# Optimization experiments

Hardware: AMD Instinct MI355X
Metric: run time of the kernel (lower is better)

The kernel has to match this reference:

```python
import jax, jax.numpy as jnp
import numpy as np

N_FEATURES = 784   # binary tabular features (MNIST-like)
Z_DIM = 64         # latent dim fed to decoder net
BX = 256           # number of data points x
BZ = 4096          # number of latent samples / components z


def setup_inputs() -> dict:
    key = jax.random.key(0)
    k1, k2, k3 = jax.random.split(key, 3)
    x = jax.random.uniform(k1, (BX, N_FEATURES), dtype=jnp.float32)  # soft targets in [0,1)
    z = jax.random.normal(k2, (BZ, Z_DIM), dtype=jnp.float32)
    # net := Linear(Z_DIM -> 2*N_FEATURES)
    W = jax.random.normal(k3, (Z_DIM, 2 * N_FEATURES), dtype=jnp.float32) * 0.05
    b = jnp.zeros((2 * N_FEATURES,), dtype=jnp.float32)
    # chain-structured CLT: root = feature 0 (parent -1), feature i's parent is i-1
    tree = jnp.concatenate([jnp.array([-1], dtype=jnp.int32),
                            jnp.arange(N_FEATURES - 1, dtype=jnp.int32)])
    return {"x": x, "z": z, "W": W, "b": b, "tree": tree}


def reference(x, z, W, b, tree):
    F = tree.shape[0]
    # net(z) -> logits_p [Bz, F, 2]
    logits_p = (z @ W + b).reshape(-1, F, 2)
    # _preprocess_logits_p: at root, copy state-1 logit into state-0 slot
    root_mask = (tree == -1)  # [F]
    lp0 = jnp.where(root_mask[None, :], logits_p[:, :, 1], logits_p[:, :, 0])
    logits_p = jnp.stack([lp0, logits_p[:, :, 1]], axis=-1)  # [Bz, F, 2]
    # parent-conditioned selector x_cond [Bx, F, 2]
    xt = x[:, tree]  # gather parent values; -1 at root wraps (same as torch)
    x_cond = jnp.stack([1.0 - xt, xt], axis=-1)
    # bce (negative binary cross-entropy = Bernoulli log-likelihood):
    #   lls[b,i,j,k] = x[b,j]*log_sigmoid(lp[i,j,k]) + (1-x[b,j])*log_sigmoid(-lp[i,j,k])
    # (x_doubled duplicates x along k, so both k slots use x[b,j])
    # Then einsum('bijk,bjk->bij', lls, x_cond).sum(-1). Distribute x_cond to
    # avoid materializing the [Bx,Bz,F,2] lls tensor (same math, fused):
    ls = jax.nn.log_sigmoid(logits_p)     # [Bz, F, 2]
    lsn = jax.nn.log_sigmoid(-logits_p)   # [Bz, F, 2]
    a = x_cond * x[:, :, None]            # [Bx, F, 2]
    c = x_cond * (1.0 - x)[:, :, None]    # [Bx, F, 2]
    log_prob_bins = (jnp.einsum('bjk,ijk->bi', a, ls)
                     + jnp.einsum('bjk,ijk->bi', c, lsn))  # [Bx, Bz]
    return log_prob_bins
```

## Files before the change

kernel.cpp:

```cpp
#include <hip/hip_runtime.h>

#define NF   784
#define ZD   64
#define BXN  256
#define BZN  4096
#define KDIM 3136
#define LCOL 1568

typedef __attribute__((ext_vector_type(8))) short bf16x8;
typedef __attribute__((ext_vector_type(4))) float f32x4;
typedef __attribute__((ext_vector_type(8))) unsigned short ushort8;
typedef __attribute__((ext_vector_type(4))) unsigned short us4;

__device__ __forceinline__ unsigned short f2bf(float f) {
  unsigned u = __float_as_uint(f);
  u += 0x7fff + ((u >> 16) & 1);
  return (unsigned short)(u >> 16);
}

__device__ __forceinline__ unsigned pkbf(float a, float b) {
  unsigned r;
  asm("v_cvt_pk_bf16_f32 %0, %1, %2" : "=v"(r) : "v"(a), "v"(b));
  return r;
}

__global__ __launch_bounds__(256) void prep(const float* __restrict__ x,
                                            const float* __restrict__ W,
                                            const int* __restrict__ tree,
                                            unsigned short* __restrict__ Amat,
                                            unsigned short* __restrict__ Wt) {
  int bid = blockIdx.x, tid = threadIdx.x;
  if (bid < 1024) {
    int b = bid >> 2;
    int j = (bid & 3) * 256 + tid;
    if (j >= NF) return;
    float xb = x[b * NF + j];
    int idx = tree[j];
    int gidx = idx < 0 ? idx + NF : idx;
    float xt = x[b * NF + gidx];
    ushort4 v;
    v.x = f2bf((1.f - xt) * xb);
    v.y = f2bf(xt * xb);
    v.z = f2bf((1.f - xt) * (1.f - xb));
    v.w = f2bf(xt * (1.f - xb));
    *(ushort4*)&Amat[(size_t)b * KDIM + 4 * j] = v;
  } else {
    int t = (bid - 1024) * 256 + tid;
    int c = t >> 4, k0 = (t & 15) * 4;
    ushort4 o;
    o.x = f2bf(W[(k0 + 0) * LCOL + c]);
    o.y = f2bf(W[(k0 + 1) * LCOL + c]);
    o.z = f2bf(W[(k0 + 2) * LCOL + c]);
    o.w = f2bf(W[(k0 + 3) * LCOL + c]);
    *(ushort4*)&Wt[c * 64 + k0] = o;
  }
}

#define LP 40
__global__ __launch_bounds__(256) void gemm_fused(const unsigned short* __restrict__ Amat,
                                                  const float* __restrict__ z,
                                                  const unsigned short* __restrict__ Wt,
                                                  const float* __restrict__ bias,
                                                  const int* __restrict__ tree,
                                                  unsigned short* __restrict__ part) {
  __shared__ unsigned short As[2][256][LP];
  __shared__ unsigned short Bs[2][64][LP];
  int bid = blockIdx.x;
  int s = bid & 7, nt = bid >> 3;
  int n0 = nt * 64;
  int kt0 = s * 12 + (s < 2 ? s : 2);
  int nsteps = (s < 2) ? 13 : 12;
  int ktend = kt0 + nsteps;
  int tid = threadIdx.x;
  int w = tid >> 6, lane = tid & 63;
  int fr = lane & 15, hi = lane >> 4, kq = hi * 8;
  int srow = tid >> 2, scol = (tid & 3) * 8;
  const unsigned short* Ag = Amat + (size_t)srow * KDIM + scol;

  const float* zpf = z + (size_t)(n0 + w * 16 + fr) * 64 + kq;
  float4 zl0 = *(const float4*)(zpf);
  float4 zl1 = *(const float4*)(zpf + 4);
  float4 zl2 = *(const float4*)(zpf + 32);
  float4 zl3 = *(const float4*)(zpf + 36);
  union { unsigned u[4]; bf16x8 v; } Z0, Z1;
  Z0.u[0] = pkbf(zl0.x, zl0.y); Z0.u[1] = pkbf(zl0.z, zl0.w);
  Z0.u[2] = pkbf(zl1.x, zl1.y); Z0.u[3] = pkbf(zl1.z, zl1.w);
  Z1.u[0] = pkbf(zl2.x, zl2.y); Z1.u[1] = pkbf(zl2.z, zl2.w);
  Z1.u[2] = pkbf(zl3.x, zl3.y); Z1.u[3] = pkbf(zl3.z, zl3.w);
  bf16x8 zf0 = Z0.v, zf1 = Z1.v;

  f32x4 acc[4][4];
#pragma unroll
  for (int m = 0; m < 4; ++m)
#pragma unroll
    for (int n = 0; n < 4; ++n) acc[m][n] = (f32x4){0.f, 0.f, 0.f, 0.f};

  const unsigned short* wp = Wt + (size_t)(kt0 * 16 + fr) * 64 + kq;
  bf16x8 wf0 = *(const bf16x8*)wp;
  bf16x8 wf1 = *(const bf16x8*)(wp + 32);
  float4 b4  = *(const float4*)&bias[kt0 * 16 + 4 * hi];
  int2   tr2 = *(const int2*)&tree[kt0 * 8 + 2 * hi];
  int k0 = kt0 * 32;
  float4 ar0 = *(const float4*)(Ag + k0);
  float4 ar1 = *(const float4*)(Ag + (size_t)64 * KDIM + k0);
  float4 ar2 = *(const float4*)(Ag + (size_t)128 * KDIM + k0);
  float4 ar3 = *(const float4*)(Ag + (size_t)192 * KDIM + k0);

  int buf = 0;
  for (int i = 0; i < nsteps; ++i) {
    int kt = kt0 + i;
    f32x4 lacc = (f32x4){0.f, 0.f, 0.f, 0.f};
    lacc = __builtin_amdgcn_mfma_f32_16x16x32_bf16(wf0, zf0, lacc, 0, 0, 0);
    lacc = __builtin_amdgcn_mfma_f32_16x16x32_bf16(wf1, zf1, lacc, 0, 0, 0);
    int ktn = (kt + 1 < ktend) ? kt + 1 : kt;
    const unsigned short* wpn = Wt + (size_t)(ktn * 16 + fr) * 64 + kq;
    bf16x8 wfn0 = *(const bf16x8*)wpn;
    bf16x8 wfn1 = *(const bf16x8*)(wpn + 32);
    float4 b4n  = *(const float4*)&bias[ktn * 16 + 4 * hi];
    int2   tr2n = *(const int2*)&tree[ktn * 8 + 2 * hi];
    int k0n = ktn * 32;
    float4 arn0 = *(const float4*)(Ag + k0n);
    float4 arn1 = *(const float4*)(Ag + (size_t)64 * KDIM + k0n);
    float4 arn2 = *(const float4*)(Ag + (size_t)128 * KDIM + k0n);
    float4 arn3 = *(const float4*)(Ag + (size_t)192 * KDIM + k0n);
    float bb[4] = { b4.x, b4.y, b4.z, b4.w };
    int tt[2] = { tr2.x, tr2.y };
    union { unsigned u[4]; ushort8 v; } V;
#pragma unroll
    for (int p = 0; p < 2; ++p) {
      float l1 = lacc[2 * p + 1] + bb[2 * p + 1];
      float l0 = (tt[p] == -1) ? l1 : (lacc[2 * p] + bb[2 * p]);
      float e0 = __expf(-fabsf(l0)); float sp0 = __logf(1.f + e0);
      float ls0 = (l0 >= 0.f) ? -sp0 : l0 - sp0;
      float e1 = __expf(-fabsf(l1)); float sp1 = __logf(1.f + e1);
      float ls1 = (l1 >= 0.f) ? -sp1 : l1 - sp1;
      V.u[2 * p + 0] = pkbf(ls0, ls1);
      V.u[2 * p + 1] = pkbf(ls0 - l0, ls1 - l1);
    }
    *(float4*)&As[buf][srow      ][scol] = ar0;
    *(float4*)&As[buf][srow +  64][scol] = ar1;
    *(float4*)&As[buf][srow + 128][scol] = ar2;
    *(float4*)&As[buf][srow + 192][scol] = ar3;
    *(ushort8*)&Bs[buf][w * 16 + fr][kq] = V.v;
    __syncthreads();
    bf16x8 a[4], b[4];
#pragma unroll
    for (int m = 0; m < 4; ++m) a[m] = *(const bf16x8*)&As[buf][w * 64 + m * 16 + fr][kq];
#pragma unroll
    for (int n = 0; n < 4; ++n) b[n] = *(const bf16x8*)&Bs[buf][n * 16 + fr][kq];
#pragma unroll
    for (int m = 0; m < 4; ++m)
#pragma unroll
      for (int n = 0; n < 4; ++n)
        acc[m][n] = __builtin_amdgcn_mfma_f32_16x16x32_bf16(a[m], b[n], acc[m][n], 0, 0, 0);
    wf0 = wfn0; wf1 = wfn1; b4 = b4n; tr2 = tr2n;
    ar0 = arn0; ar1 = arn1; ar2 = arn2; ar3 = arn3;
    buf ^= 1;
  }
  int col = lane & 15, rq = hi * 4;
  unsigned short* Pp = part + (size_t)s * (256 * 4096) + (size_t)(w * 64) * 4096 + n0;
#pragma unroll
  for (int m = 0; m < 4; ++m)
#pragma unroll
    for (int n = 0; n < 4; ++n)
#pragma unroll
      for (int r = 0; r < 4; ++r)
        __builtin_nontemporal_store(f2bf(acc[m][n][r]),
                                    &Pp[(m * 16 + rq + r) * 4096 + n * 16 + col]);
}

__global__ __launch_bounds__(256) void reduce8(const unsigned short* __restrict__ part,
                                               float* __restrict__ out) {
  int t = blockIdx.x * 256 + threadIdx.x;
  f32x4 s = (f32x4){0.f, 0.f, 0.f, 0.f};
#pragma unroll
  for (int q = 0; q < 8; ++q) {
    const us4* p = (const us4*)&part[(size_t)q * (256 * 4096) + (size_t)t * 4];
    us4 v = __builtin_nontemporal_load(p);
    s[0] += __uint_as_float((unsigned)v[0] << 16);
    s[1] += __uint_as_float((unsigned)v[1] << 16);
    s[2] += __uint_as_float((unsigned)v[2] << 16);
    s[3] += __uint_as_float((unsigned)v[3] << 16);
  }
  f32x4* o = (f32x4*)&out[(size_t)t * 4];
  __builtin_nontemporal_store(s, o);
}

extern "C" void kernel_launch(void* const* d_in, const int* in_sizes, int n_in,
                              void* d_out, int out_size, void* d_ws, size_t ws_size,
                              hipStream_t stream) {
  const float* x    = (const float*)d_in[0];
  const float* z    = (const float*)d_in[1];
  const float* W    = (const float*)d_in[2];
  const float* bias = (const float*)d_in[3];
  const int*   tree = (const int*)d_in[4];
  float* out = (float*)d_out;

  unsigned short* Amat = (unsigned short*)d_ws;
  unsigned short* Wt   = (unsigned short*)((char*)d_ws + 1605632);
  unsigned short* part = (unsigned short*)((char*)d_ws + 1806336);

  prep<<<dim3(1122), 256, 0, stream>>>(x, W, tree, Amat, Wt);
  gemm_fused<<<dim3(512), 256, 0, stream>>>(Amat, z, Wt, bias, tree, part);
  reduce8<<<dim3(1024), 256, 0, stream>>>(part, out);
}
```

Measured before the change: 37.06 us.

## Double gemm block to 512 threads, halving per-wave M tile with producer waves

```diff
diff --git a/kernel.cpp b/kernel.cpp
--- a/kernel.cpp
+++ b/kernel.cpp
@@ -57,12 +57,12 @@
 }
 
 #define LP 40
-__global__ __launch_bounds__(256) void gemm_fused(const unsigned short* __restrict__ Amat,
-                                                  const float* __restrict__ z,
-                                                  const unsigned short* __restrict__ Wt,
-                                                  const float* __restrict__ bias,
-                                                  const int* __restrict__ tree,
-                                                  unsigned short* __restrict__ part) {
+__global__ __launch_bounds__(512, 4) void gemm_fused(const unsigned short* __restrict__ Amat,
+                                                     const float* __restrict__ z,
+                                                     const unsigned short* __restrict__ Wt,
+                                                     const float* __restrict__ bias,
+                                                     const int* __restrict__ tree,
+                                                     unsigned short* __restrict__ part) {
   __shared__ unsigned short As[2][256][LP];
   __shared__ unsigned short Bs[2][64][LP];
   int bid = blockIdx.x;
@@ -74,93 +74,105 @@
   int tid = threadIdx.x;
   int w = tid >> 6, lane = tid & 63;
   int fr = lane & 15, hi = lane >> 4, kq = hi * 8;
-  int srow = tid >> 2, scol = (tid & 3) * 8;
+  int srow = tid >> 1, scol = (tid & 1) * 8;
   const unsigned short* Ag = Amat + (size_t)srow * KDIM + scol;
-
-  const float* zpf = z + (size_t)(n0 + w * 16 + fr) * 64 + kq;
-  float4 zl0 = *(const float4*)(zpf);
-  float4 zl1 = *(const float4*)(zpf + 4);
-  float4 zl2 = *(const float4*)(zpf + 32);
-  float4 zl3 = *(const float4*)(zpf + 36);
-  union { unsigned u[4]; bf16x8 v; } Z0, Z1;
-  Z0.u[0] = pkbf(zl0.x, zl0.y); Z0.u[1] = pkbf(zl0.z, zl0.w);
-  Z0.u[2] = pkbf(zl1.x, zl1.y); Z0.u[3] = pkbf(zl1.z, zl1.w);
-  Z1.u[0] = pkbf(zl2.x, zl2.y); Z1.u[1] = pkbf(zl2.z, zl2.w);
-  Z1.u[2] = pkbf(zl3.x, zl3.y); Z1.u[3] = pkbf(zl3.z, zl3.w);
-  bf16x8 zf0 = Z0.v, zf1 = Z1.v;
-
-  f32x4 acc[4][4];
-#pragma unroll
-  for (int m = 0; m < 4; ++m)
+  bool prod = (w < 4);
+
+  bf16x8 zf0 = {}, zf1 = {};
+  if (prod) {
+    const float* zpf = z + (size_t)(n0 + w * 16 + fr) * 64 + kq;
+    float4 zl0 = *(const float4*)(zpf);
+    float4 zl1 = *(const float4*)(zpf + 4);
+    float4 zl2 = *(const float4*)(zpf + 32);
+    float4 zl3 = *(const float4*)(zpf + 36);
+    union { unsigned u[4]; bf16x8 v; } Z0, Z1;
+    Z0.u[0] = pkbf(zl0.x, zl0.y); Z0.u[1] = pkbf(zl0.z, zl0.w);
+    Z0.u[2] = pkbf(zl1.x, zl1.y); Z0.u[3] = pkbf(zl1.z, zl1.w);
+    Z1.u[0] = pkbf(zl2.x, zl2.y); Z1.u[1] = pkbf(zl2.z, zl2.w);
+    Z1.u[2] = pkbf(zl3.x, zl3.y); Z1.u[3] = pkbf(zl3.z, zl3.w);
+    zf0 = Z0.v; zf1 = Z1.v;
+  }
+
+  f32x4 acc[2][4];
+#pragma unroll
+  for (int m = 0; m < 2; ++m)
 #pragma unroll
     for (int n = 0; n < 4; ++n) acc[m][n] = (f32x4){0.f, 0.f, 0.f, 0.f};
 
-  const unsigned short* wp = Wt + (size_t)(kt0 * 16 + fr) * 64 + kq;
-  bf16x8 wf0 = *(const bf16x8*)wp;
-  bf16x8 wf1 = *(const bf16x8*)(wp + 32);
-  float4 b4  = *(const float4*)&bias[kt0 * 16 + 4 * hi];
-  int2   tr2 = *(const int2*)&tree[kt0 * 8 + 2 * hi];
+  bf16x8 wf0 = {}, wf1 = {};
+  float4 b4 = {};
+  int2 tr2 = {};
+  if (prod) {
+    const unsigned short* wp = Wt + (size_t)(kt0 * 16 + fr) * 64 + kq;
+    wf0 = *(const bf16x8*)wp;
+    wf1 = *(const bf16x8*)(wp + 32);
+    b4  = *(const float4*)&bias[kt0 * 16 + 4 * hi];
+    tr2 = *(const int2*)&tree[kt0 * 8 + 2 * hi];
+  }
   int k0 = kt0 * 32;
   float4 ar0 = *(const float4*)(Ag + k0);
-  float4 ar1 = *(const float4*)(Ag + (size_t)64 * KDIM + k0);
-  float4 ar2 = *(const float4*)(Ag + (size_t)128 * KDIM + k0);
-  float4 ar3 = *(const float4*)(Ag + (size_t)192 * KDIM + k0);
+  float4 ar1 = *(const float4*)(Ag + 16 + k0);
 
   int buf = 0;
   for (int i = 0; i < nsteps; ++i) {
     int kt = kt0 + i;
+    int ktn = (kt + 1 < ktend) ? kt + 1 : kt;
     f32x4 lacc = (f32x4){0.f, 0.f, 0.f, 0.f};
-    lacc = __builtin_amdgcn_mfma_f32_16x16x32_bf16(wf0, zf0, lacc, 0, 0, 0);
-    lacc = __builtin_amdgcn_mfma_f32_16x16x32_bf16(wf1, zf1, lacc, 0, 0, 0);
-    int ktn = (kt + 1 < ktend) ? kt + 1 : kt;
-    const unsigned short* wpn = Wt + (size_t)(ktn * 16 + fr) * 64 + kq;
-    bf16x8 wfn0 = *(const bf16x8*)wpn;
-    bf16x8 wfn1 = *(const bf16x8*)(wpn + 32);
-    float4 b4n  = *(const float4*)&bias[ktn * 16 + 4 * hi];
-    int2   tr2n = *(const int2*)&tree[ktn * 8 + 2 * hi];
+    if (prod) {
+      lacc = __builtin_amdgcn_mfma_f32_16x16x32_bf16(wf0, zf0, lacc, 0, 0, 0);
+      lacc = __builtin_amdgcn_mfma_f32_16x16x32_bf16(wf1, zf1, lacc, 0, 0, 0);
+    }
+    bf16x8 wfn0 = {}, wfn1 = {};
+    float4 b4n = {};
+    int2 tr2n = {};
+    if (prod) {
+      const unsigned short* wpn = Wt + (size_t)(ktn * 16 + fr) * 64 + kq;
+      wfn0 = *(const bf16x8*)wpn;
+      wfn1 = *(const bf16x8*)(wpn + 32);
+      b4n  = *(const float4*)&bias[ktn * 16 + 4 * hi];
+      tr2n = *(const int2*)&tree[ktn * 8 + 2 * hi];
+    }
     int k0n = ktn * 32;
     float4 arn0 = *(const float4*)(Ag + k0n);
-    float4 arn1 = *(const float4*)(Ag + (size_t)64 * KDIM + k0n);
-    float4 arn2 = *(const float4*)(Ag + (size_t)128 * KDIM + k0n);
-    float4 arn3 = *(const float4*)(Ag + (size_t)192 * KDIM + k0n);
-    float bb[4] = { b4.x, b4.y, b4.z, b4.w };
-    int tt[2] = { tr2.x, tr2.y };
-    union { unsigned u[4]; ushort8 v; } V;
-#pragma unroll
-    for (int p = 0; p < 2; ++p) {
-      float l1 = lacc[2 * p + 1] + bb[2 * p + 1];
-      float l0 = (tt[p] == -1) ? l1 : (lacc[2 * p] + bb[2 * p]);
-      float e0 = __expf(-fabsf(l0)); float sp0 = __logf(1.f + e0);
-      float ls0 = (l0 >= 0.f) ? -sp0 : l0 - sp0;
-      float e1 = __expf(-fabsf(l1)); float sp1 = __logf(1.f + e1);
-      float ls1 = (l1 >= 0.f) ? -sp1 : l1 - sp1;
-      V.u[2 * p + 0] = pkbf(ls0, ls1);
-      V.u[2 * p + 1] = pkbf(ls0 - l0, ls1 - l1);
-    }
-    *(float4*)&As[buf][srow      ][scol] = ar0;
-    *(float4*)&As[buf][srow +  64][scol] = ar1;
-    *(float4*)&As[buf][srow + 128][scol] = ar2;
-    *(float4*)&As[buf][srow + 192][scol] = ar3;
-    *(ushort8*)&Bs[buf][w * 16 + fr][kq] = V.v;
+    float4 arn1 = *(const float4*)(Ag + 16 + k0n);
+    if (prod) {
+      float bb[4] = { b4.x, b4.y, b4.z, b4.w };
+      int tt[2] = { tr2.x, tr2.y };
+      union { unsigned u[4]; ushort8 v; } V;
+#pragma unroll
+      for (int p = 0; p < 2; ++p) {
+        float l1 = lacc[2 * p + 1] + bb[2 * p + 1];
+        float l0 = (tt[p] == -1) ? l1 : (lacc[2 * p] + bb[2 * p]);
+        float e0 = __expf(-fabsf(l0)); float sp0 = __logf(1.f + e0);
+        float ls0 = (l0 >= 0.f) ? -sp0 : l0 - sp0;
+        float e1 = __expf(-fabsf(l1)); float sp1 = __logf(1.f + e1);
+        float ls1 = (l1 >= 0.f) ? -sp1 : l1 - sp1;
+        V.u[2 * p + 0] = pkbf(ls0, ls1);
+        V.u[2 * p + 1] = pkbf(ls0 - l0, ls1 - l1);
+      }
+      *(ushort8*)&Bs[buf][w * 16 + fr][kq] = V.v;
+    }
+    *(float4*)&As[buf][srow][scol     ] = ar0;
+    *(float4*)&As[buf][srow][scol + 16] = ar1;
     __syncthreads();
-    bf16x8 a[4], b[4];
-#pragma unroll
-    for (int m = 0; m < 4; ++m) a[m] = *(const bf16x8*)&As[buf][w * 64 + m * 16 + fr][kq];
+    bf16x8 a0 = *(const bf16x8*)&As[buf][w * 32 + fr][kq];
+    bf16x8 a1 = *(const bf16x8*)&As[buf][w * 32 + 16 + fr][kq];
+    bf16x8 b[4];
 #pragma unroll
     for (int n = 0; n < 4; ++n) b[n] = *(const bf16x8*)&Bs[buf][n * 16 + fr][kq];
 #pragma unroll
-    for (int m = 0; m < 4; ++m)
-#pragma unroll
-      for (int n = 0; n < 4; ++n)
-        acc[m][n] = __builtin_amdgcn_mfma_f32_16x16x32_bf16(a[m], b[n], acc[m][n], 0, 0, 0);
+    for (int n = 0; n < 4; ++n) {
+      acc[0][n] = __builtin_amdgcn_mfma_f32_16x16x32_bf16(a0, b[n], acc[0][n], 0, 0, 0);
+      acc[1][n] = __builtin_amdgcn_mfma_f32_16x16x32_bf16(a1, b[n], acc[1][n], 0, 0, 0);
+    }
     wf0 = wfn0; wf1 = wfn1; b4 = b4n; tr2 = tr2n;
-    ar0 = arn0; ar1 = arn1; ar2 = arn2; ar3 = arn3;
+    ar0 = arn0; ar1 = arn1;
     buf ^= 1;
   }
   int col = lane & 15, rq = hi * 4;
-  unsigned short* Pp = part + (size_t)s * (256 * 4096) + (size_t)(w * 64) * 4096 + n0;
-#pragma unroll
-  for (int m = 0; m < 4; ++m)
+  unsigned short* Pp = part + (size_t)s * (256 * 4096) + (size_t)(w * 32) * 4096 + n0;
+#pragma unroll
+  for (int m = 0; m < 2; ++m)
 #pragma unroll
     for (int n = 0; n < 4; ++n)
 #pragma unroll
@@ -201,6 +213,6 @@
   unsigned short* part = (unsigned short*)((char*)d_ws + 1806336);
 
   prep<<<dim3(1122), 256, 0, stream>>>(x, W, tree, Amat, Wt);
-  gemm_fused<<<dim3(512), 256, 0, stream>>>(Amat, z, Wt, bias, tree, part);
+  gemm_fused<<<dim3(512), 512, 0, stream>>>(Amat, z, Wt, bias, tree, part);
   reduce8<<<dim3(1024), 256, 0, stream>>>(part, out);
 }
```

Measured after the change: 41.18 us. 1.11x slower.

## Software-pipeline decoder logits and log-sigmoid one K-step ahead of main MFMA

Applied to the files above, without the earlier changes.

```diff
diff --git a/kernel.cpp b/kernel.cpp
--- a/kernel.cpp
+++ b/kernel.cpp
@@ -95,37 +95,19 @@
 #pragma unroll
     for (int n = 0; n < 4; ++n) acc[m][n] = (f32x4){0.f, 0.f, 0.f, 0.f};
 
-  const unsigned short* wp = Wt + (size_t)(kt0 * 16 + fr) * 64 + kq;
-  bf16x8 wf0 = *(const bf16x8*)wp;
-  bf16x8 wf1 = *(const bf16x8*)(wp + 32);
-  float4 b4  = *(const float4*)&bias[kt0 * 16 + 4 * hi];
-  int2   tr2 = *(const int2*)&tree[kt0 * 8 + 2 * hi];
-  int k0 = kt0 * 32;
-  float4 ar0 = *(const float4*)(Ag + k0);
-  float4 ar1 = *(const float4*)(Ag + (size_t)64 * KDIM + k0);
-  float4 ar2 = *(const float4*)(Ag + (size_t)128 * KDIM + k0);
-  float4 ar3 = *(const float4*)(Ag + (size_t)192 * KDIM + k0);
-
-  int buf = 0;
-  for (int i = 0; i < nsteps; ++i) {
-    int kt = kt0 + i;
+  ushort8 V;
+  {
+    const unsigned short* wpp = Wt + (size_t)(kt0 * 16 + fr) * 64 + kq;
+    bf16x8 pwf0 = *(const bf16x8*)wpp;
+    bf16x8 pwf1 = *(const bf16x8*)(wpp + 32);
+    float4 pb4  = *(const float4*)&bias[kt0 * 16 + 4 * hi];
+    int2   ptr2 = *(const int2*)&tree[kt0 * 8 + 2 * hi];
     f32x4 lacc = (f32x4){0.f, 0.f, 0.f, 0.f};
-    lacc = __builtin_amdgcn_mfma_f32_16x16x32_bf16(wf0, zf0, lacc, 0, 0, 0);
-    lacc = __builtin_amdgcn_mfma_f32_16x16x32_bf16(wf1, zf1, lacc, 0, 0, 0);
-    int ktn = (kt + 1 < ktend) ? kt + 1 : kt;
-    const unsigned short* wpn = Wt + (size_t)(ktn * 16 + fr) * 64 + kq;
-    bf16x8 wfn0 = *(const bf16x8*)wpn;
-    bf16x8 wfn1 = *(const bf16x8*)(wpn + 32);
-    float4 b4n  = *(const float4*)&bias[ktn * 16 + 4 * hi];
-    int2   tr2n = *(const int2*)&tree[ktn * 8 + 2 * hi];
-    int k0n = ktn * 32;
-    float4 arn0 = *(const float4*)(Ag + k0n);
-    float4 arn1 = *(const float4*)(Ag + (size_t)64 * KDIM + k0n);
-    float4 arn2 = *(const float4*)(Ag + (size_t)128 * KDIM + k0n);
-    float4 arn3 = *(const float4*)(Ag + (size_t)192 * KDIM + k0n);
-    float bb[4] = { b4.x, b4.y, b4.z, b4.w };
-    int tt[2] = { tr2.x, tr2.y };
-    union { unsigned u[4]; ushort8 v; } V;
+    lacc = __builtin_amdgcn_mfma_f32_16x16x32_bf16(pwf0, zf0, lacc, 0, 0, 0);
+    lacc = __builtin_amdgcn_mfma_f32_16x16x32_bf16(pwf1, zf1, lacc, 0, 0, 0);
+    float bb[4] = { pb4.x, pb4.y, pb4.z, pb4.w };
+    int tt[2] = { ptr2.x, ptr2.y };
+    union { unsigned u[4]; ushort8 v; } VV;
 #pragma unroll
     for (int p = 0; p < 2; ++p) {
       float l1 = lacc[2 * p + 1] + bb[2 * p + 1];
@@ -134,25 +116,72 @@
       float ls0 = (l0 >= 0.f) ? -sp0 : l0 - sp0;
       float e1 = __expf(-fabsf(l1)); float sp1 = __logf(1.f + e1);
       float ls1 = (l1 >= 0.f) ? -sp1 : l1 - sp1;
-      V.u[2 * p + 0] = pkbf(ls0, ls1);
-      V.u[2 * p + 1] = pkbf(ls0 - l0, ls1 - l1);
+      VV.u[2 * p + 0] = pkbf(ls0, ls1);
+      VV.u[2 * p + 1] = pkbf(ls0 - l0, ls1 - l1);
     }
+    V = VV.v;
+  }
+  int k0 = kt0 * 32;
+  float4 ar0 = *(const float4*)(Ag + k0);
+  float4 ar1 = *(const float4*)(Ag + (size_t)64 * KDIM + k0);
+  float4 ar2 = *(const float4*)(Ag + (size_t)128 * KDIM + k0);
+  float4 ar3 = *(const float4*)(Ag + (size_t)192 * KDIM + k0);
+  int kt1 = (kt0 + 1 < ktend) ? kt0 + 1 : ktend - 1;
+  const unsigned short* wp1 = Wt + (size_t)(kt1 * 16 + fr) * 64 + kq;
+  bf16x8 wf0 = *(const bf16x8*)wp1;
+  bf16x8 wf1 = *(const bf16x8*)(wp1 + 32);
+  float4 b4  = *(const float4*)&bias[kt1 * 16 + 4 * hi];
+  int2   tr2 = *(const int2*)&tree[kt1 * 8 + 2 * hi];
+
+  int buf = 0;
+  for (int i = 0; i < nsteps; ++i) {
+    int kt = kt0 + i;
+    int ktn  = (kt + 1 < ktend) ? kt + 1 : ktend - 1;
+    int ktnn = (kt + 2 < ktend) ? kt + 2 : ktend - 1;
     *(float4*)&As[buf][srow      ][scol] = ar0;
     *(float4*)&As[buf][srow +  64][scol] = ar1;
     *(float4*)&As[buf][srow + 128][scol] = ar2;
     *(float4*)&As[buf][srow + 192][scol] = ar3;
-    *(ushort8*)&Bs[buf][w * 16 + fr][kq] = V.v;
+    *(ushort8*)&Bs[buf][w * 16 + fr][kq] = V;
+    int k0n = ktn * 32;
+    float4 arn0 = *(const float4*)(Ag + k0n);
+    float4 arn1 = *(const float4*)(Ag + (size_t)64 * KDIM + k0n);
+    float4 arn2 = *(const float4*)(Ag + (size_t)128 * KDIM + k0n);
+    float4 arn3 = *(const float4*)(Ag + (size_t)192 * KDIM + k0n);
     __syncthreads();
     bf16x8 a[4], b[4];
 #pragma unroll
     for (int m = 0; m < 4; ++m) a[m] = *(const bf16x8*)&As[buf][w * 64 + m * 16 + fr][kq];
 #pragma unroll
     for (int n = 0; n < 4; ++n) b[n] = *(const bf16x8*)&Bs[buf][n * 16 + fr][kq];
+    f32x4 lacc = (f32x4){0.f, 0.f, 0.f, 0.f};
+    lacc = __builtin_amdgcn_mfma_f32_16x16x32_bf16(wf0, zf0, lacc, 0, 0, 0);
+    lacc = __builtin_amdgcn_mfma_f32_16x16x32_bf16(wf1, zf1, lacc, 0, 0, 0);
+    const unsigned short* wpn = Wt + (size_t)(ktnn * 16 + fr) * 64 + kq;
+    bf16x8 wfn0 = *(const bf16x8*)wpn;
+    bf16x8 wfn1 = *(const bf16x8*)(wpn + 32);
+    float4 b4n  = *(const float4*)&bias[ktnn * 16 + 4 * hi];
+    int2   tr2n = *(const int2*)&tree[ktnn * 8 + 2 * hi];
+    float bb[4] = { b4.x, b4.y, b4.z, b4.w };
+    int tt[2] = { tr2.x, tr2.y };
+    union { unsigned u[4]; ushort8 v; } VV;
+#pragma unroll
+    for (int p = 0; p < 2; ++p) {
+      float l1 = lacc[2 * p + 1] + bb[2 * p + 1];
+      float l0 = (tt[p] == -1) ? l1 : (lacc[2 * p] + bb[2 * p]);
+      float e0 = __expf(-fabsf(l0)); float sp0 = __logf(1.f + e0);
+      float ls0 = (l0 >= 0.f) ? -sp0 : l0 - sp0;
+      float e1 = __expf(-fabsf(l1)); float sp1 = __logf(1.f + e1);
+      float ls1 = (l1 >= 0.f) ? -sp1 : l1 - sp1;
+      VV.u[2 * p + 0] = pkbf(ls0, ls1);
+      VV.u[2 * p + 1] = pkbf(ls0 - l0, ls1 - l1);
+    }
 #pragma unroll
     for (int m = 0; m < 4; ++m)
 #pragma unroll
       for (int n = 0; n < 4; ++n)
         acc[m][n] = __builtin_amdgcn_mfma_f32_16x16x32_bf16(a[m], b[n], acc[m][n], 0, 0, 0);
+    V = VV.v;
     wf0 = wfn0; wf1 = wfn1; b4 = b4n; tr2 = tr2n;
     ar0 = arn0; ar1 = arn1; ar2 = arn2; ar3 = arn3;
     buf ^= 1;
```

Result: no change. 36.95 us, median of 2 (-0.3%).
